# Kernel optimization log

Measured on AMD Instinct MI355X. Metric: run time of the kernel, lower is better.

Reference implementation:

```python
import jax, jax.numpy as jnp
import numpy as np

TREND_SCALING = 0.6
DETAIL_PRESERVATION = 0.85
SPIKE_THRESHOLD = 3.5
SPIKE_DAMPING = 0.35
ITERATIONS = 2
EPS = 1e-6


def _smooth(x, kernel):
    # x: [B, C, L], kernel: [1, 1, W] (normalized box filter)
    W = kernel.shape[-1]
    pad = W // 2
    xp = jnp.pad(x, ((0, 0), (0, 0), (pad, pad)), mode='reflect')
    C = x.shape[1]
    w = jnp.broadcast_to(kernel, (C, 1, W))  # depthwise weight [C, 1, W]
    return jax.lax.conv_general_dilated(
        xp, w, window_strides=(1,), padding='VALID',
        dimension_numbers=('NCH', 'OIH', 'NCH'), feature_group_count=C)


def setup_inputs() -> dict:
    key = jax.random.key(0)
    x = jax.random.normal(key, (16, 32, 65536), dtype=jnp.float32)
    # buffers from __init__ with base_window=5
    detail_kernel = jnp.ones((1, 1, 5), dtype=jnp.float32) / 5.0
    trend_kernel = jnp.ones((1, 1, 11), dtype=jnp.float32) / 11.0
    return {"x": x, "detail_kernel": detail_kernel, "trend_kernel": trend_kernel}


def reference(x, detail_kernel, trend_kernel):
    current = x.astype(jnp.float32)
    for _ in range(ITERATIONS):
        trend = _smooth(current, trend_kernel)
        local = _smooth(current, detail_kernel)
        residual = current - local
        # torch .std uses Bessel's correction (ddof=1)
        scale = jnp.maximum(jnp.std(residual, axis=-1, keepdims=True, ddof=1), EPS)
        threshold = scale * SPIKE_THRESHOLD
        residual = jnp.where(jnp.abs(residual) > threshold,
                             residual * SPIKE_DAMPING, residual)
        residual = residual * DETAIL_PRESERVATION
        combined = (1.0 - TREND_SCALING) * local + TREND_SCALING * trend
        current = combined + residual
    return current
```

## Files before the change

kernel.cpp:

```cpp
#include <hip/hip_runtime.h>
#include <math.h>

#define LROW   65536
#define NROWS  512
#define NT     512
#define NW     (NT / 64)
#define NCHK   16
#define CHUNK  4096
#define EPC    (CHUNK / NT)
#define HB     10
#define NELEM  (CHUNK + 2 * HB)

#define TREND_SCALING       0.6f
#define DETAIL_PRESERVATION 0.85f
#define SPIKE_THRESHOLD     3.5f
#define SPIKE_DAMPING       0.35f
#define EPSV                1e-6f

__device__ __forceinline__ int sw(int i) { return i + (i >> 4); }

__device__ __forceinline__ float block_thresh(double s, double q,
                                              double* __restrict__ wred,
                                              const int tid) {
#pragma unroll
    for (int off = 32; off > 0; off >>= 1) {
        s += __shfl_xor(s, off);
        q += __shfl_xor(q, off);
    }
    if ((tid & 63) == 0) {
        wred[tid >> 6] = s;
        wred[(tid >> 6) + NW] = q;
    }
    __syncthreads();
    double S = 0.0, Q = 0.0;
#pragma unroll
    for (int w = 0; w < NW; w++) { S += wred[w]; Q += wred[w + NW]; }
    const double N = (double)LROW;
    double var = (Q - S * S / N) / (N - 1.0);
    if (var < 0.0) var = 0.0;
    return fmaxf((float)sqrt(var), EPSV) * SPIKE_THRESHOLD;
}

__global__ __launch_bounds__(NT) void k_fused(const float* __restrict__ x,
                                              float* __restrict__ out,
                                              const float* __restrict__ k5,
                                              const float* __restrict__ k11) {
    __shared__ float buf[NELEM + (NELEM >> 4) + 4];
    __shared__ double wred[2 * NW];

    const int row = blockIdx.x;
    const int tid = threadIdx.x;
    const size_t rowBase = (size_t)row * LROW;
    const float w5 = k5[0];
    const float w11 = k11[0];
    const int E0 = tid * EPC;

    float4 r0, r1;
    float hreg;
#define LOAD_CHUNK(c)                                                         \
    {                                                                         \
        const float4* s4 = (const float4*)(x + rowBase + (c) * CHUNK);        \
        r0 = s4[tid];                                                         \
        r1 = s4[tid + NT];                                                    \
        if (tid < 2 * HB) {                                                   \
            int g = (tid < HB) ? ((c) * CHUNK - HB + tid)                     \
                               : ((c) * CHUNK + CHUNK + tid - HB);            \
            g = (g < 0) ? -g : (g >= LROW ? 2 * LROW - 2 - g : g);            \
            hreg = x[rowBase + g];                                            \
        }                                                                     \
    }
#define STORE_CHUNK()                                                         \
    {                                                                         \
        int l0 = tid * 4 + HB;                                                \
        buf[sw(l0)] = r0.x; buf[sw(l0 + 1)] = r0.y;                           \
        buf[sw(l0 + 2)] = r0.z; buf[sw(l0 + 3)] = r0.w;                       \
        int l1 = (tid + NT) * 4 + HB;                                         \
        buf[sw(l1)] = r1.x; buf[sw(l1 + 1)] = r1.y;                           \
        buf[sw(l1 + 2)] = r1.z; buf[sw(l1 + 3)] = r1.w;                       \
        if (tid < 2 * HB) {                                                   \
            int l = (tid < HB) ? tid : (CHUNK + HB + tid - HB);               \
            buf[sw(l)] = hreg;                                                \
        }                                                                     \
    }

    double s = 0.0, q = 0.0;
    LOAD_CHUNK(0)
#pragma unroll 1
    for (int c = 0; c < NCHK; ++c) {
        __syncthreads();
        STORE_CHUNK()
        if (c < NCHK - 1) LOAD_CHUNK(c + 1)
        __syncthreads();
        float v[EPC + 4];
#pragma unroll
        for (int m = 0; m < EPC + 4; m++) v[m] = buf[sw(E0 + (HB - 2) + m)];
#pragma unroll
        for (int k = 0; k < EPC; k++) {
            float lac = 0.f;
#pragma unroll
            for (int d = 0; d < 5; d++) lac = fmaf(v[k + d], w5, lac);
            float r = v[k + 2] - lac;
            s += (double)r;
            q += (double)r * (double)r;
        }
    }
    const float th1 = block_thresh(s, q, wred, tid);

    s = 0.0; q = 0.0;
    LOAD_CHUNK(0)
#pragma unroll 1
    for (int c = 0; c < NCHK; ++c) {
        __syncthreads();
        STORE_CHUNK()
        if (c < NCHK - 1) LOAD_CHUNK(c + 1)
        __syncthreads();
        float xw[EPC + 14];
#pragma unroll
        for (int m = 0; m < EPC + 14; m++) xw[m] = buf[sw(E0 + (HB - 7) + m)];
        float y[EPC + 4];
#pragma unroll
        for (int j = 0; j < EPC + 4; j++) {
            float lac = 0.f, tac = 0.f;
#pragma unroll
            for (int d = 0; d < 5; d++) lac = fmaf(xw[j + 3 + d], w5, lac);
#pragma unroll
            for (int d = 0; d < 11; d++) tac = fmaf(xw[j + d], w11, tac);
            float cur = xw[j + 5];
            float r = cur - lac;
            r = (fabsf(r) > th1) ? r * SPIKE_DAMPING : r;
            float comb = (1.0f - TREND_SCALING) * lac + TREND_SCALING * tac;
            y[j] = comb + DETAIL_PRESERVATION * r;
        }
#pragma unroll
        for (int k = 0; k < EPC; k++) {
            float lac = 0.f;
#pragma unroll
            for (int d = 0; d < 5; d++) lac = fmaf(y[k + d], w5, lac);
            float r = y[k + 2] - lac;
            s += (double)r;
            q += (double)r * (double)r;
        }
    }
    const float th2 = block_thresh(s, q, wred, tid);

    LOAD_CHUNK(0)
#pragma unroll 1
    for (int c = 0; c < NCHK; ++c) {
        __syncthreads();
        STORE_CHUNK()
        if (c < NCHK - 1) LOAD_CHUNK(c + 1)
        __syncthreads();
        float xw[EPC + 20];
#pragma unroll
        for (int m = 0; m < EPC + 20; m++) xw[m] = buf[sw(E0 + m)];
        float y[EPC + 10];
#pragma unroll
        for (int j = 0; j < EPC + 10; j++) {
            float lac = 0.f, tac = 0.f;
#pragma unroll
            for (int d = 0; d < 5; d++) lac = fmaf(xw[j + 3 + d], w5, lac);
#pragma unroll
            for (int d = 0; d < 11; d++) tac = fmaf(xw[j + d], w11, tac);
            float cur = xw[j + 5];
            float r = cur - lac;
            r = (fabsf(r) > th1) ? r * SPIKE_DAMPING : r;
            float comb = (1.0f - TREND_SCALING) * lac + TREND_SCALING * tac;
            y[j] = comb + DETAIL_PRESERVATION * r;
        }
        float o[EPC];
#pragma unroll
        for (int k = 0; k < EPC; k++) {
            float lac = 0.f, tac = 0.f;
#pragma unroll
            for (int d = 0; d < 5; d++) lac = fmaf(y[k + 3 + d], w5, lac);
#pragma unroll
            for (int d = 0; d < 11; d++) tac = fmaf(y[k + d], w11, tac);
            float cur = y[k + 5];
            float r = cur - lac;
            r = (fabsf(r) > th2) ? r * SPIKE_DAMPING : r;
            float comb = (1.0f - TREND_SCALING) * lac + TREND_SCALING * tac;
            o[k] = comb + DETAIL_PRESERVATION * r;
        }
        float4* d4 = (float4*)(out + rowBase + c * CHUNK + E0);
        d4[0] = make_float4(o[0], o[1], o[2], o[3]);
        d4[1] = make_float4(o[4], o[5], o[6], o[7]);
    }
#undef LOAD_CHUNK
#undef STORE_CHUNK
}

extern "C" void kernel_launch(void* const* d_in, const int* in_sizes, int n_in,
                              void* d_out, int out_size, void* d_ws, size_t ws_size,
                              hipStream_t stream) {
    (void)in_sizes; (void)n_in; (void)out_size; (void)d_ws; (void)ws_size;
    const float* x = (const float*)d_in[0];
    const float* k5 = (const float*)d_in[1];
    const float* k11 = (const float*)d_in[2];
    float* out = (float*)d_out;

    hipLaunchKernelGGL(k_fused, dim3(NROWS), dim3(NT), 0, stream, x, out, k5, k11);
}
```

Before: 323.0 us.

## Double-buffer LDS chunks, stage intermediate y in shared memory, use float4 XOR-swizzled LDS

The input chunk buffer is double-buffered so one barrier per chunk is removed. Shared memory becomes float4 with an XOR swizzle, so window reads are vector LDS loads instead of scalar ones. The first-iteration output y is computed once per element and shared through an LDS buffer with halo fixups, replacing the per-thread recomputation of overlapping y windows in passes two and three. The cost is extra LDS, an added barrier between the y and consumer stages, and more complex halo handling by a few threads.

```diff
diff --git a/kernel.cpp b/kernel.cpp
--- a/kernel.cpp
+++ b/kernel.cpp
@@ -7,9 +7,11 @@
 #define NW     (NT / 64)
 #define NCHK   16
 #define CHUNK  4096
-#define EPC    (CHUNK / NT)
-#define HB     10
-#define NELEM  (CHUNK + 2 * HB)
+#define EPC    8
+#define HBX    12
+#define HBY    8
+#define NFXP   1032
+#define NFYP   1032
 
 #define TREND_SCALING       0.6f
 #define DETAIL_PRESERVATION 0.85f
@@ -17,7 +19,14 @@
 #define SPIKE_DAMPING       0.35f
 #define EPSV                1e-6f
 
-__device__ __forceinline__ int sw(int i) { return i + (i >> 4); }
+__device__ __forceinline__ int swz(int I) { return I ^ ((I >> 3) & 7); }
+
+__device__ __forceinline__ float ldsGet(const float4* B, int i) {
+    return ((const float*)&B[swz(i >> 2)])[i & 3];
+}
+__device__ __forceinline__ void ldsPut(float4* B, int i, float v) {
+    ((float*)&B[swz(i >> 2)])[i & 3] = v;
+}
 
 __device__ __forceinline__ float block_thresh(double s, double q,
                                               double* __restrict__ wred,
@@ -41,152 +50,174 @@
     return fmaxf((float)sqrt(var), EPSV) * SPIKE_THRESHOLD;
 }
 
+__device__ __forceinline__ float y_of(const float* xa, float w5, float w11,
+                                      float th1) {
+    float lac = 0.f, tac = 0.f;
+#pragma unroll
+    for (int d = 0; d < 5; d++) lac = fmaf(xa[3 + d], w5, lac);
+#pragma unroll
+    for (int d = 0; d < 11; d++) tac = fmaf(xa[d], w11, tac);
+    float cur = xa[5];
+    float r = cur - lac;
+    r = (fabsf(r) > th1) ? r * SPIKE_DAMPING : r;
+    float comb = (1.0f - TREND_SCALING) * lac + TREND_SCALING * tac;
+    return comb + DETAIL_PRESERVATION * r;
+}
+
 __global__ __launch_bounds__(NT) void k_fused(const float* __restrict__ x,
                                               float* __restrict__ out,
                                               const float* __restrict__ k5,
                                               const float* __restrict__ k11) {
-    __shared__ float buf[NELEM + (NELEM >> 4) + 4];
+    __shared__ float4 bx[2][NFXP];
+    __shared__ float4 by[NFYP];
     __shared__ double wred[2 * NW];
 
     const int row = blockIdx.x;
-    const int tid = threadIdx.x;
+    const int t = threadIdx.x;
     const size_t rowBase = (size_t)row * LROW;
     const float w5 = k5[0];
     const float w11 = k11[0];
-    const int E0 = tid * EPC;
+    const int E0 = t * EPC;
+    const float4* X4 = (const float4*)(x + rowBase);
 
     float4 r0, r1;
     float hreg;
-#define LOAD_CHUNK(c)                                                         \
+
+#define LOADC(c)                                                              \
     {                                                                         \
-        const float4* s4 = (const float4*)(x + rowBase + (c) * CHUNK);        \
-        r0 = s4[tid];                                                         \
-        r1 = s4[tid + NT];                                                    \
-        if (tid < 2 * HB) {                                                   \
-            int g = (tid < HB) ? ((c) * CHUNK - HB + tid)                     \
-                               : ((c) * CHUNK + CHUNK + tid - HB);            \
+        r0 = X4[(c) * 1024 + t];                                              \
+        r1 = X4[(c) * 1024 + t + NT];                                         \
+        if (t < 2 * HBX) {                                                    \
+            int i = (t < HBX) ? t : CHUNK + t;                                \
+            int g = (c) * CHUNK + i - HBX;                                    \
             g = (g < 0) ? -g : (g >= LROW ? 2 * LROW - 2 - g : g);            \
             hreg = x[rowBase + g];                                            \
         }                                                                     \
     }
-#define STORE_CHUNK()                                                         \
+#define STOREC(B)                                                             \
     {                                                                         \
-        int l0 = tid * 4 + HB;                                                \
-        buf[sw(l0)] = r0.x; buf[sw(l0 + 1)] = r0.y;                           \
-        buf[sw(l0 + 2)] = r0.z; buf[sw(l0 + 3)] = r0.w;                       \
-        int l1 = (tid + NT) * 4 + HB;                                         \
-        buf[sw(l1)] = r1.x; buf[sw(l1 + 1)] = r1.y;                           \
-        buf[sw(l1 + 2)] = r1.z; buf[sw(l1 + 3)] = r1.w;                       \
-        if (tid < 2 * HB) {                                                   \
-            int l = (tid < HB) ? tid : (CHUNK + HB + tid - HB);               \
-            buf[sw(l)] = hreg;                                                \
+        (B)[swz(t + 3)] = r0;                                                 \
+        (B)[swz(t + NT + 3)] = r1;                                            \
+        if (t < 2 * HBX) {                                                    \
+            int i = (t < HBX) ? t : CHUNK + t;                                \
+            ldsPut((B), i, hreg);                                             \
+        }                                                                     \
+    }
+#define MAKE_Y(B, th1v)                                                       \
+    {                                                                         \
+        float xw[24];                                                         \
+        _Pragma("unroll") for (int j = 0; j < 6; ++j) {                       \
+            float4 wv = (B)[swz(2 * t + 1 + j)];                              \
+            xw[4 * j] = wv.x; xw[4 * j + 1] = wv.y;                           \
+            xw[4 * j + 2] = wv.z; xw[4 * j + 3] = wv.w;                       \
+        }                                                                     \
+        float yo[EPC];                                                        \
+        _Pragma("unroll") for (int k = 0; k < EPC; ++k)                       \
+            yo[k] = y_of(&xw[k + 3], w5, w11, (th1v));                        \
+        by[swz(2 * t + 2)] = make_float4(yo[0], yo[1], yo[2], yo[3]);         \
+        by[swz(2 * t + 3)] = make_float4(yo[4], yo[5], yo[6], yo[7]);         \
+        if (t < 10) {                                                         \
+            int p = (t < 5) ? (t - 5) : (CHUNK + t - 5);                      \
+            float xa[11];                                                     \
+            _Pragma("unroll") for (int j = 0; j < 11; ++j)                    \
+                xa[j] = ldsGet((B), p - 5 + j + HBX);                         \
+            ldsPut(by, p + HBY, y_of(xa, w5, w11, (th1v)));                   \
         }                                                                     \
     }
 
     double s = 0.0, q = 0.0;
-    LOAD_CHUNK(0)
+    LOADC(0)
 #pragma unroll 1
     for (int c = 0; c < NCHK; ++c) {
-        __syncthreads();
-        STORE_CHUNK()
-        if (c < NCHK - 1) LOAD_CHUNK(c + 1)
-        __syncthreads();
-        float v[EPC + 4];
-#pragma unroll
-        for (int m = 0; m < EPC + 4; m++) v[m] = buf[sw(E0 + (HB - 2) + m)];
-#pragma unroll
-        for (int k = 0; k < EPC; k++) {
+        float4* B = bx[c & 1];
+        STOREC(B)
+        if (c + 1 < NCHK) LOADC(c + 1)
+        __syncthreads();
+        float v[16];
+#pragma unroll
+        for (int j = 0; j < 4; ++j) {
+            float4 wv = B[swz(2 * t + 2 + j)];
+            v[4 * j] = wv.x; v[4 * j + 1] = wv.y;
+            v[4 * j + 2] = wv.z; v[4 * j + 3] = wv.w;
+        }
+#pragma unroll
+        for (int k = 0; k < EPC; ++k) {
             float lac = 0.f;
 #pragma unroll
-            for (int d = 0; d < 5; d++) lac = fmaf(v[k + d], w5, lac);
-            float r = v[k + 2] - lac;
+            for (int d = 0; d < 5; ++d) lac = fmaf(v[k + 2 + d], w5, lac);
+            float r = v[k + 4] - lac;
             s += (double)r;
             q += (double)r * (double)r;
         }
     }
-    const float th1 = block_thresh(s, q, wred, tid);
+    const float th1 = block_thresh(s, q, wred, t);
 
     s = 0.0; q = 0.0;
-    LOAD_CHUNK(0)
+    LOADC(0)
 #pragma unroll 1
     for (int c = 0; c < NCHK; ++c) {
-        __syncthreads();
-        STORE_CHUNK()
-        if (c < NCHK - 1) LOAD_CHUNK(c + 1)
-        __syncthreads();
-        float xw[EPC + 14];
-#pragma unroll
-        for (int m = 0; m < EPC + 14; m++) xw[m] = buf[sw(E0 + (HB - 7) + m)];
-        float y[EPC + 4];
-#pragma unroll
-        for (int j = 0; j < EPC + 4; j++) {
-            float lac = 0.f, tac = 0.f;
-#pragma unroll
-            for (int d = 0; d < 5; d++) lac = fmaf(xw[j + 3 + d], w5, lac);
-#pragma unroll
-            for (int d = 0; d < 11; d++) tac = fmaf(xw[j + d], w11, tac);
-            float cur = xw[j + 5];
-            float r = cur - lac;
-            r = (fabsf(r) > th1) ? r * SPIKE_DAMPING : r;
-            float comb = (1.0f - TREND_SCALING) * lac + TREND_SCALING * tac;
-            y[j] = comb + DETAIL_PRESERVATION * r;
-        }
-#pragma unroll
-        for (int k = 0; k < EPC; k++) {
+        float4* B = bx[c & 1];
+        STOREC(B)
+        if (c + 1 < NCHK) LOADC(c + 1)
+        __syncthreads();
+        MAKE_Y(B, th1)
+        __syncthreads();
+        float yw[16];
+#pragma unroll
+        for (int j = 0; j < 4; ++j) {
+            float4 wv = by[swz(2 * t + 1 + j)];
+            yw[4 * j] = wv.x; yw[4 * j + 1] = wv.y;
+            yw[4 * j + 2] = wv.z; yw[4 * j + 3] = wv.w;
+        }
+#pragma unroll
+        for (int k = 0; k < EPC; ++k) {
             float lac = 0.f;
 #pragma unroll
-            for (int d = 0; d < 5; d++) lac = fmaf(y[k + d], w5, lac);
-            float r = y[k + 2] - lac;
+            for (int d = 0; d < 5; ++d) lac = fmaf(yw[k + 2 + d], w5, lac);
+            float r = yw[k + 4] - lac;
             s += (double)r;
             q += (double)r * (double)r;
         }
     }
-    const float th2 = block_thresh(s, q, wred, tid);
-
-    LOAD_CHUNK(0)
+    const float th2 = block_thresh(s, q, wred, t);
+
+    LOADC(0)
 #pragma unroll 1
     for (int c = 0; c < NCHK; ++c) {
-        __syncthreads();
-        STORE_CHUNK()
-        if (c < NCHK - 1) LOAD_CHUNK(c + 1)
-        __syncthreads();
-        float xw[EPC + 20];
-#pragma unroll
-        for (int m = 0; m < EPC + 20; m++) xw[m] = buf[sw(E0 + m)];
-        float y[EPC + 10];
-#pragma unroll
-        for (int j = 0; j < EPC + 10; j++) {
+        float4* B = bx[c & 1];
+        STOREC(B)
+        if (c + 1 < NCHK) LOADC(c + 1)
+        __syncthreads();
+        MAKE_Y(B, th1)
+        __syncthreads();
+        float yw[24];
+#pragma unroll
+        for (int j = 0; j < 6; ++j) {
+            float4 wv = by[swz(2 * t + j)];
+            yw[4 * j] = wv.x; yw[4 * j + 1] = wv.y;
+            yw[4 * j + 2] = wv.z; yw[4 * j + 3] = wv.w;
+        }
+        float o[EPC];
+#pragma unroll
+        for (int k = 0; k < EPC; ++k) {
             float lac = 0.f, tac = 0.f;
 #pragma unroll
-            for (int d = 0; d < 5; d++) lac = fmaf(xw[j + 3 + d], w5, lac);
-#pragma unroll
-            for (int d = 0; d < 11; d++) tac = fmaf(xw[j + d], w11, tac);
-            float cur = xw[j + 5];
-            float r = cur - lac;
-            r = (fabsf(r) > th1) ? r * SPIKE_DAMPING : r;
-            float comb = (1.0f - TREND_SCALING) * lac + TREND_SCALING * tac;
-            y[j] = comb + DETAIL_PRESERVATION * r;
-        }
-        float o[EPC];
-#pragma unroll
-        for (int k = 0; k < EPC; k++) {
-            float lac = 0.f, tac = 0.f;
-#pragma unroll
-            for (int d = 0; d < 5; d++) lac = fmaf(y[k + 3 + d], w5, lac);
-#pragma unroll
-            for (int d = 0; d < 11; d++) tac = fmaf(y[k + d], w11, tac);
-            float cur = y[k + 5];
+            for (int d = 0; d < 5; ++d) lac = fmaf(yw[k + 6 + d], w5, lac);
+#pragma unroll
+            for (int d = 0; d < 11; ++d) tac = fmaf(yw[k + 3 + d], w11, tac);
+            float cur = yw[k + 8];
             float r = cur - lac;
             r = (fabsf(r) > th2) ? r * SPIKE_DAMPING : r;
             float comb = (1.0f - TREND_SCALING) * lac + TREND_SCALING * tac;
             o[k] = comb + DETAIL_PRESERVATION * r;
         }
-        float4* d4 = (float4*)(out + rowBase + c * CHUNK + E0);
-        d4[0] = make_float4(o[0], o[1], o[2], o[3]);
-        d4[1] = make_float4(o[4], o[5], o[6], o[7]);
-    }
-#undef LOAD_CHUNK
-#undef STORE_CHUNK
+        float4* O4 = (float4*)(out + rowBase + c * CHUNK + E0);
+        O4[0] = make_float4(o[0], o[1], o[2], o[3]);
+        O4[1] = make_float4(o[4], o[5], o[6], o[7]);
+    }
+#undef LOADC
+#undef STOREC
+#undef MAKE_Y
 }
 
 extern "C" void kernel_launch(void* const* d_in, const int* in_sizes, int n_in,
```

Result: slower. 336.6 us (+4.2%).
